# Kernel tuning notes

Hardware: AMD Instinct MI355X
Metric: run time of the kernel (lower is better)

## Reference

```python
import jax, jax.numpy as jnp
import numpy as np

LN_EPS = 1e-5

def setup_inputs() -> dict:
    key = jax.random.key(0)
    ks = jax.random.split(key, 12)
    B, S, D = 4, 2048, 1024
    s = 1.0 / np.sqrt(D)
    return {
        "query": jax.random.normal(ks[0], (B, S, D), jnp.float32),
        "key_in": jax.random.normal(ks[1], (B, S, D), jnp.float32),
        "value": jax.random.normal(ks[2], (B, S, D), jnp.float32),
        "Wq": jax.random.normal(ks[3], (D, D), jnp.float32) * s,
        "bq": jax.random.normal(ks[4], (D,), jnp.float32) * s,
        "Wk": jax.random.normal(ks[5], (D, D), jnp.float32) * s,
        "bk": jax.random.normal(ks[6], (D,), jnp.float32) * s,
        "Wv": jax.random.normal(ks[7], (D, D), jnp.float32) * s,
        "bv": jax.random.normal(ks[8], (D,), jnp.float32) * s,
        "gamma": jnp.ones((D,), jnp.float32),
        "beta": jnp.zeros((D,), jnp.float32),
    }

def reference(query, key_in, value, Wq, bq, Wk, bk, Wv, bv, gamma, beta):
    # Linear projections (torch Linear: x @ W^T + b; here W stored as [in,out])
    q = jnp.einsum('bsd,df->bsf', query, Wq) + bq
    k = jnp.einsum('bsd,df->bsf', key_in, Wk) + bk
    v = jnp.einsum('bsd,df->bsf', value, Wv) + bv
    # Attention: note NO 1/sqrt(d) scaling, single head (faithful to source)
    attn = jnp.einsum('bqd,bkd->bqk', q, k)          # [B,S,S]
    probs = jax.nn.softmax(attn, axis=-1)
    result = jnp.einsum('bqk,bkd->bqd', probs, v)     # [B,S,D]
    # Residual + LayerNorm
    x = result + query
    mu = jnp.mean(x, axis=-1, keepdims=True)
    var = jnp.mean((x - mu) ** 2, axis=-1, keepdims=True)
    return (x - mu) * jax.lax.rsqrt(var + LN_EPS) * gamma + beta
```

## Files before the change

### kernel.cpp

```cpp
#include <hip/hip_runtime.h>
#include <hip/hip_bf16.h>
#include <cstdint>


typedef unsigned short u16;
typedef unsigned int   u32;
typedef _Float16 f16;
typedef f16   f16x8  __attribute__((ext_vector_type(8)));
typedef f16   f16x4  __attribute__((ext_vector_type(4)));
typedef float f32x4  __attribute__((ext_vector_type(4)));

#define DEV __device__ __forceinline__

DEV void gld_lds16(const f16* g, char* l){
  __builtin_amdgcn_global_load_lds(
      (const __attribute__((address_space(1))) u32*)(uintptr_t)g,
      (__attribute__((address_space(3))) u32*)(u32)(uintptr_t)l, 16, 0, 0);
}

#define MFMA_(av, bv, ci, cj) \
  acc[ci][cj] = __builtin_amdgcn_mfma_f32_16x16x32_f16(av, bv, acc[ci][cj], 0, 0, 0)

DEV void gemm_core(const f16* __restrict__ A, int lda,
                   const f16* __restrict__ B, int ldb,
                   int nt, char* smem, f32x4 (&acc)[8][4])
{
  const int tid  = threadIdx.x;
  const int lane = tid & 63;
  const int wv   = tid >> 6;
  const int wm   = wv >> 2, wn = wv & 3;
  const int lr   = lane & 15, lq = lane >> 4;

  const int ob0 = tid * 16;
  const int ob1 = ob0 + 8192;
  const int r0  = ob0 >> 7, r1 = ob1 >> 7;
  const int sl0 = ((ob0 >> 4) & 7) ^ (r0 & 7);
  const int sl1 = ((ob1 >> 4) & 7) ^ (r1 & 7);
  const f16* src[8];
  src[0] = A + (size_t)r0 * lda + sl0 * 8;
  src[1] = A + (size_t)r1 * lda + sl1 * 8;
  src[2] = B + (size_t)r0 * ldb + sl0 * 8;
  src[3] = B + (size_t)r1 * ldb + sl1 * 8;
  src[4] = A + (size_t)(128 + r0) * lda + sl0 * 8;
  src[5] = A + (size_t)(128 + r1) * lda + sl1 * 8;
  src[6] = B + (size_t)(128 + r0) * ldb + sl0 * 8;
  src[7] = B + (size_t)(128 + r1) * ldb + sl1 * 8;

  const int rA  = (wm * 16 + lr) << 7;
  const int rB  = (wn * 16 + lr) << 7;
  const int sk0 = ((lq ^ (lane & 7)) << 4);
  const int sk1 = (((4 | lq) ^ (lane & 7)) << 4);

#pragma unroll
  for (int i = 0; i < 8; i++)
#pragma unroll
    for (int j = 0; j < 4; j++) acc[i][j] = (f32x4){0.f, 0.f, 0.f, 0.f};

  gld_lds16(src[0], smem +     0 + ob0); src[0] += 64;
  gld_lds16(src[1], smem +     0 + ob1); src[1] += 64;
  gld_lds16(src[2], smem + 32768 + ob0); src[2] += 64;
  gld_lds16(src[3], smem + 32768 + ob1); src[3] += 64;
  gld_lds16(src[4], smem + 16384 + ob0); src[4] += 64;
  gld_lds16(src[5], smem + 16384 + ob1); src[5] += 64;
  gld_lds16(src[6], smem + 49152 + ob0); src[6] += 64;
  gld_lds16(src[7], smem + 49152 + ob1); src[7] += 64;

  for (int t = 0; t < nt; ++t){
    char* bufc  = smem + ((t & 1) << 16);
    char* stash = smem + (((t & 1) ^ 1) << 16);
    const bool more = (t + 1 < nt);

    f16x8 a0[4], a1[4], b0[2], b1[2], b2[2], b3[2];

    if (more){ gld_lds16(src[0], stash + 0 + ob0); src[0] += 64; }
    if (more) asm volatile("s_waitcnt vmcnt(5)\ns_barrier" ::: "memory");
    else      asm volatile("s_waitcnt vmcnt(4)\ns_barrier" ::: "memory");
#pragma unroll
    for (int i = 0; i < 4; i++) a0[i] = *(const f16x8*)(bufc + (i << 12) + rA + sk0);
    b0[0] = *(const f16x8*)(bufc + 32768 +    0 + rB + sk0);
    b0[1] = *(const f16x8*)(bufc + 32768 + 8192 + rB + sk0);
    __builtin_amdgcn_s_setprio(1);
#pragma unroll
    for (int i = 0; i < 4; i++){ MFMA_(a0[i], b0[0], i, 0); MFMA_(a0[i], b0[1], i, 1); }
    __builtin_amdgcn_s_setprio(0);

    if (more){ gld_lds16(src[1], stash + 0 + ob1); src[1] += 64; }
#pragma unroll
    for (int i = 0; i < 4; i++) a1[i] = *(const f16x8*)(bufc + (i << 12) + rA + sk1);
    b1[0] = *(const f16x8*)(bufc + 32768 +    0 + rB + sk1);
    b1[1] = *(const f16x8*)(bufc + 32768 + 8192 + rB + sk1);
    __builtin_amdgcn_s_setprio(1);
#pragma unroll
    for (int i = 0; i < 4; i++){ MFMA_(a1[i], b1[0], i, 0); MFMA_(a1[i], b1[1], i, 1); }
    __builtin_amdgcn_s_setprio(0);

    if (more){ gld_lds16(src[2], stash + 32768 + ob0); src[2] += 64; }
    if (more) asm volatile("s_waitcnt vmcnt(3)\ns_barrier" ::: "memory");
    else      asm volatile("s_waitcnt vmcnt(0)\ns_barrier" ::: "memory");
    b2[0] = *(const f16x8*)(bufc + 49152 +    0 + rB + sk0);
    b2[1] = *(const f16x8*)(bufc + 49152 + 8192 + rB + sk0);
    __builtin_amdgcn_s_setprio(1);
#pragma unroll
    for (int i = 0; i < 4; i++){ MFMA_(a0[i], b2[0], i, 2); MFMA_(a0[i], b2[1], i, 3); }
    __builtin_amdgcn_s_setprio(0);

    if (more){ gld_lds16(src[3], stash + 32768 + ob1); src[3] += 64; }
    b3[0] = *(const f16x8*)(bufc + 49152 +    0 + rB + sk1);
    b3[1] = *(const f16x8*)(bufc + 49152 + 8192 + rB + sk1);
    __builtin_amdgcn_s_setprio(1);
#pragma unroll
    for (int i = 0; i < 4; i++){ MFMA_(a1[i], b3[0], i, 2); MFMA_(a1[i], b3[1], i, 3); }
    __builtin_amdgcn_s_setprio(0);

    if (more){ gld_lds16(src[4], stash + 16384 + ob0); src[4] += 64; }
#pragma unroll
    for (int i = 0; i < 4; i++) a0[i] = *(const f16x8*)(bufc + 16384 + (i << 12) + rA + sk0);
    __builtin_amdgcn_s_setprio(1);
#pragma unroll
    for (int i = 0; i < 4; i++){ MFMA_(a0[i], b0[0], 4 + i, 0); MFMA_(a0[i], b0[1], 4 + i, 1); }
    __builtin_amdgcn_s_setprio(0);

    if (more){ gld_lds16(src[5], stash + 16384 + ob1); src[5] += 64; }
#pragma unroll
    for (int i = 0; i < 4; i++) a1[i] = *(const f16x8*)(bufc + 16384 + (i << 12) + rA + sk1);
    __builtin_amdgcn_s_setprio(1);
#pragma unroll
    for (int i = 0; i < 4; i++){ MFMA_(a1[i], b1[0], 4 + i, 0); MFMA_(a1[i], b1[1], 4 + i, 1); }
    __builtin_amdgcn_s_setprio(0);

    if (more){ gld_lds16(src[6], stash + 49152 + ob0); src[6] += 64; }
    __builtin_amdgcn_s_setprio(1);
#pragma unroll
    for (int i = 0; i < 4; i++){ MFMA_(a0[i], b2[0], 4 + i, 2); MFMA_(a0[i], b2[1], 4 + i, 3); }
    __builtin_amdgcn_s_setprio(0);

    if (more){ gld_lds16(src[7], stash + 49152 + ob1); src[7] += 64; }
    __builtin_amdgcn_s_setprio(1);
#pragma unroll
    for (int i = 0; i < 4; i++){ MFMA_(a1[i], b3[0], 4 + i, 2); MFMA_(a1[i], b3[1], 4 + i, 3); }
    __builtin_amdgcn_s_setprio(0);
  }
}

__global__ __launch_bounds__(512, 2) void proj8p(
    const f16* __restrict__ xq, const f16* __restrict__ xk, const f16* __restrict__ xv,
    const f16* __restrict__ wq, const f16* __restrict__ wk, const f16* __restrict__ wv,
    const float* __restrict__ bq, const float* __restrict__ bk, const float* __restrict__ bv,
    f16* __restrict__ oq, f16* __restrict__ ok, f16* __restrict__ ovT)
{
  __shared__ char smem[131072];
  const int z  = blockIdx.z;
  const int m0 = blockIdx.y * 256, n0 = blockIdx.x * 256;
  const f16* A = (z == 0 ? xq : z == 1 ? xk : xv) + (size_t)m0 * 1024;
  const f16* B = (z == 0 ? wq : z == 1 ? wk : wv) + (size_t)n0 * 1024;
  const float* bias = (z == 0 ? bq : z == 1 ? bk : bv);

  f32x4 acc[8][4];
  gemm_core(A, 1024, B, 1024, 16, smem, acc);

  const int lane = threadIdx.x & 63;
  const int wv_  = threadIdx.x >> 6;
  const int wm = wv_ >> 2, wn = wv_ & 3;
  const int lr = lane & 15, rj = (lane >> 4) * 4;

  if (z < 2){
    f16* o = z ? ok : oq;
#pragma unroll
    for (int i = 0; i < 8; i++)
#pragma unroll
      for (int j = 0; j < 4; j++){
        int row = m0 + i * 32 + wm * 16 + rj;
        int col = n0 + j * 64 + wn * 16 + lr;
        float bvl = bias[col];
#pragma unroll
        for (int r = 0; r < 4; r++)
          o[(size_t)(row + r) * 1024 + col] = (f16)(acc[i][j][r] + bvl);
      }
  } else {
#pragma unroll
    for (int i = 0; i < 8; i++)
#pragma unroll
      for (int j = 0; j < 4; j++){
        int row = m0 + i * 32 + wm * 16 + rj;
        int col = n0 + j * 64 + wn * 16 + lr;
        float bvl = bias[col];
        f16x4 tv;
#pragma unroll
        for (int r = 0; r < 4; r++) tv[r] = (f16)(acc[i][j][r] + bvl);
        *(f16x4*)(ovT + (size_t)col * 8192 + row) = tv;
      }
  }
}

__global__ __launch_bounds__(512, 2) void qk8p(
    const f16* __restrict__ q, const f16* __restrict__ k, float* __restrict__ Sout)
{
  __shared__ char smem[131072];
  const int z  = blockIdx.z;
  const int m0 = blockIdx.y * 256, n0 = blockIdx.x * 256;
  const f16* A = q + (size_t)z * 2048 * 1024 + (size_t)m0 * 1024;
  const f16* B = k + (size_t)z * 2048 * 1024 + (size_t)n0 * 1024;

  f32x4 acc[8][4];
  gemm_core(A, 1024, B, 1024, 16, smem, acc);

  const int lane = threadIdx.x & 63;
  const int wv_  = threadIdx.x >> 6;
  const int wm = wv_ >> 2, wn = wv_ & 3;
  const int lr = lane & 15, rj = (lane >> 4) * 4;
  float* o = Sout + (size_t)z * 2048 * 2048;
#pragma unroll
  for (int i = 0; i < 8; i++)
#pragma unroll
    for (int j = 0; j < 4; j++){
      int row = m0 + i * 32 + wm * 16 + rj;
      int col = n0 + j * 64 + wn * 16 + lr;
#pragma unroll
      for (int r = 0; r < 4; r++)
        o[(size_t)(row + r) * 2048 + col] = acc[i][j][r];
    }
}

__global__ __launch_bounds__(512, 2) void pv8p(
    const f16* __restrict__ P, const f16* __restrict__ vT, float* __restrict__ O)
{
  __shared__ char smem[131072];
  const int z  = blockIdx.z;
  const int zb = z >> 1, h = z & 1;
  const int m0 = blockIdx.y * 256, n0 = blockIdx.x * 256;
  const f16* A = P  + (size_t)zb * 2048 * 2048 + (size_t)m0 * 2048 + h * 1024;
  const f16* B = vT + (size_t)n0 * 8192 + (size_t)zb * 2048 + h * 1024;

  f32x4 acc[8][4];
  gemm_core(A, 2048, B, 8192, 16, smem, acc);

  const int lane = threadIdx.x & 63;
  const int wv_  = threadIdx.x >> 6;
  const int wm = wv_ >> 2, wn = wv_ & 3;
  const int lr = lane & 15, rj = (lane >> 4) * 4;
  float* o = O + (size_t)h * 8388608 + (size_t)zb * 2048 * 1024;
#pragma unroll
  for (int i = 0; i < 8; i++)
#pragma unroll
    for (int j = 0; j < 4; j++){
      int row = m0 + i * 32 + wm * 16 + rj;
      int col = n0 + j * 64 + wn * 16 + lr;
#pragma unroll
      for (int r = 0; r < 4; r++)
        o[(size_t)(row + r) * 1024 + col] = acc[i][j][r];
    }
}

__global__ __launch_bounds__(256) void cvt_f32_f16(const float* __restrict__ x,
                                                   f16* __restrict__ y, int n){
  int i = (blockIdx.x * 256 + threadIdx.x) * 8;
  if (i >= n) return;
  float4 a = *(const float4*)(x + i);
  float4 b = *(const float4*)(x + i + 4);
  f16x8 v;
  v[0]=(f16)a.x; v[1]=(f16)a.y; v[2]=(f16)a.z; v[3]=(f16)a.w;
  v[4]=(f16)b.x; v[5]=(f16)b.y; v[6]=(f16)b.z; v[7]=(f16)b.w;
  *(f16x8*)(y + i) = v;
}

__global__ __launch_bounds__(256) void transpose_cvt_w(const float* __restrict__ W,
                                                       f16* __restrict__ T, int D){
  __shared__ float t[32][33];
  int tx = threadIdx.x & 31, ty = threadIdx.x >> 5;
  int bx = blockIdx.x * 32, by = blockIdx.y * 32;
#pragma unroll
  for (int j = 0; j < 4; j++) t[ty + j*8][tx] = W[(size_t)(by + ty + j*8) * D + bx + tx];
  __syncthreads();
#pragma unroll
  for (int j = 0; j < 4; j++){
    float v = t[tx][ty + j*8];
    T[(size_t)(bx + ty + j*8) * D + by + tx] = (f16)v;
  }
}

DEV float wred_max(float v){
#pragma unroll
  for (int o = 32; o; o >>= 1) v = fmaxf(v, __shfl_xor(v, o));
  return v;
}
DEV float wred_sum(float v){
#pragma unroll
  for (int o = 32; o; o >>= 1) v += __shfl_xor(v, o);
  return v;
}

__global__ __launch_bounds__(256) void softmax_rows(const float* __restrict__ S, f16* __restrict__ P){
  const int row = blockIdx.x;
  const int tid = threadIdx.x;
  const float* x = S + (size_t)row * 2048 + tid * 8;
  f16* p = P + (size_t)row * 2048 + tid * 8;
  float4 a = *(const float4*)x, b = *(const float4*)(x + 4);
  float v[8] = {a.x, a.y, a.z, a.w, b.x, b.y, b.z, b.w};
  __shared__ float red[4];

  float m = v[0];
#pragma unroll
  for (int j = 1; j < 8; j++) m = fmaxf(m, v[j]);
  m = wred_max(m);
  if ((tid & 63) == 0) red[tid >> 6] = m;
  __syncthreads();
  m = fmaxf(fmaxf(red[0], red[1]), fmaxf(red[2], red[3]));

  float s = 0.f;
#pragma unroll
  for (int j = 0; j < 8; j++){ v[j] = __expf(v[j] - m); s += v[j]; }
  s = wred_sum(s);
  __syncthreads();
  if ((tid & 63) == 0) red[tid >> 6] = s;
  __syncthreads();
  s = red[0] + red[1] + red[2] + red[3];

  float inv = 1.f / s;
  f16x8 o;
#pragma unroll
  for (int j = 0; j < 8; j++) o[j] = (f16)(v[j] * inv);
  *(f16x8*)p = o;
}

__global__ __launch_bounds__(256) void resid_ln2(const float* __restrict__ O0,
                                                 const float* __restrict__ O1,
                                                 const float* __restrict__ query,
                                                 const float* __restrict__ gamma,
                                                 const float* __restrict__ beta,
                                                 float* __restrict__ out){
  const int row = blockIdx.x;
  const int tid = threadIdx.x;
  const size_t base = (size_t)row * 1024 + tid * 4;
  float4 o4 = *(const float4*)(O0 + base);
  float4 p4 = *(const float4*)(O1 + base);
  float4 q4 = *(const float4*)(query + base);
  float x[4] = {o4.x + p4.x + q4.x, o4.y + p4.y + q4.y,
                o4.z + p4.z + q4.z, o4.w + p4.w + q4.w};
  float s = 0.f, ss = 0.f;
#pragma unroll
  for (int j = 0; j < 4; j++){ s += x[j]; ss += x[j] * x[j]; }

  __shared__ float red[4];
  s = wred_sum(s);
  if ((tid & 63) == 0) red[tid >> 6] = s;
  __syncthreads();
  s = red[0] + red[1] + red[2] + red[3];
  ss = wred_sum(ss);
  __syncthreads();
  if ((tid & 63) == 0) red[tid >> 6] = ss;
  __syncthreads();
  ss = red[0] + red[1] + red[2] + red[3];

  float mu = s * (1.f / 1024.f);
  float var = ss * (1.f / 1024.f) - mu * mu;
  float rs = rsqrtf(var + 1e-5f);
  float4 g4 = *(const float4*)(gamma + tid * 4);
  float4 b4 = *(const float4*)(beta + tid * 4);
  float4 r;
  r.x = (x[0] - mu) * rs * g4.x + b4.x;
  r.y = (x[1] - mu) * rs * g4.y + b4.y;
  r.z = (x[2] - mu) * rs * g4.z + b4.z;
  r.w = (x[3] - mu) * rs * g4.w + b4.w;
  *(float4*)(out + base) = r;
}

extern "C" void kernel_launch(void* const* d_in, const int* in_sizes, int n_in,
                              void* d_out, int out_size, void* d_ws, size_t ws_size,
                              hipStream_t stream){
  const float* query  = (const float*)d_in[0];
  const float* key_in = (const float*)d_in[1];
  const float* value  = (const float*)d_in[2];
  const float* Wq = (const float*)d_in[3];
  const float* bq = (const float*)d_in[4];
  const float* Wk = (const float*)d_in[5];
  const float* bk = (const float*)d_in[6];
  const float* Wv = (const float*)d_in[7];
  const float* bv = (const float*)d_in[8];
  const float* gamma = (const float*)d_in[9];
  const float* beta  = (const float*)d_in[10];

  const int B = 4, S = 2048, D = 1024;
  const int M = B * S;
  const size_t MB = 1ull << 20;
  char* ws = (char*)d_ws;

  f16* qf16 = (f16*)(ws + 0);
  f16* kf16 = (f16*)(ws + 16 * MB);
  f16* vT   = (f16*)(ws + 32 * MB);
  f16* wt_q = (f16*)(ws + 48 * MB);
  f16* wt_k = (f16*)(ws + 50 * MB);
  f16* wt_v = (f16*)(ws + 52 * MB);
  float* Obuf = (float*)(ws + 54 * MB);
  f16* xq   = (f16*)(ws + 118 * MB);
  f16* xk   = (f16*)(ws + 134 * MB);
  f16* xv   = (f16*)(ws + 150 * MB);
  float* Sbuf = (float*)(ws + 118 * MB);
  f16*   Pbuf = (f16*)(ws + 182 * MB);

  dim3 blk(256);
  const int nElem = M * D;

  cvt_f32_f16<<<nElem / 2048, blk, 0, stream>>>(query,  xq, nElem);
  cvt_f32_f16<<<nElem / 2048, blk, 0, stream>>>(key_in, xk, nElem);
  cvt_f32_f16<<<nElem / 2048, blk, 0, stream>>>(value,  xv, nElem);

  dim3 tg(32, 32);
  transpose_cvt_w<<<tg, blk, 0, stream>>>(Wq, wt_q, D);
  transpose_cvt_w<<<tg, blk, 0, stream>>>(Wk, wt_k, D);
  transpose_cvt_w<<<tg, blk, 0, stream>>>(Wv, wt_v, D);

  proj8p<<<dim3(4, 32, 3), dim3(512), 0, stream>>>(xq, xk, xv, wt_q, wt_k, wt_v,
                                                   bq, bk, bv, qf16, kf16, vT);

  qk8p<<<dim3(8, 8, 4), dim3(512), 0, stream>>>(qf16, kf16, Sbuf);

  softmax_rows<<<M, blk, 0, stream>>>(Sbuf, Pbuf);

  pv8p<<<dim3(4, 8, 8), dim3(512), 0, stream>>>(Pbuf, vT, Obuf);

  resid_ln2<<<M, blk, 0, stream>>>(Obuf, Obuf + 8388608, query, gamma, beta, (float*)d_out);
}
```

Measured before the change: 209.0 us.

## Swizzle GEMM block order across XCDs, peel last k-tile, merge prep launches

Each GEMM kernel now remaps its linear block id with an XCD-aware swizzle, so consecutive logical tiles land on the same chiplet and share L2 reuse of A/B panels. The k-loop body is templated on whether a prefetch follows, and the last iteration is peeled so the runtime 'more' branches drop out of the hot loop. The three f32->f16 convert launches and the three weight-transpose launches are each merged into one launch with a z dimension, which cuts launch overhead. The swizzle assumes the block count divides evenly by 8.

```diff
diff --git a/kernel.cpp b/kernel.cpp
--- a/kernel.cpp
+++ b/kernel.cpp
@@ -18,8 +18,90 @@
       (__attribute__((address_space(3))) u32*)(u32)(uintptr_t)l, 16, 0, 0);
 }
 
+DEV int swz_lid(){
+  int lid = (blockIdx.z * gridDim.y + blockIdx.y) * gridDim.x + blockIdx.x;
+  int cpx = (gridDim.x * gridDim.y * gridDim.z) >> 3;
+  return (lid & 7) * cpx + (lid >> 3);
+}
+
 #define MFMA_(av, bv, ci, cj) \
   acc[ci][cj] = __builtin_amdgcn_mfma_f32_16x16x32_f16(av, bv, acc[ci][cj], 0, 0, 0)
+
+template<bool MORE>
+DEV void ktile_body(const f16* (&src)[8], char* bufc, char* stash,
+                    int ob0, int ob1, int rA, int rB, int sk0, int sk1,
+                    f32x4 (&acc)[8][4])
+{
+  f16x8 a0[4], a1[4], b0[2], b1[2], b2[2], b3[2];
+
+  if (MORE){ gld_lds16(src[0], stash + 0 + ob0); src[0] += 64; }
+  if (MORE) asm volatile("s_waitcnt vmcnt(5)\ns_barrier" ::: "memory");
+  else      asm volatile("s_waitcnt vmcnt(4)\ns_barrier" ::: "memory");
+#pragma unroll
+  for (int i = 0; i < 4; i++) a0[i] = *(const f16x8*)(bufc + (i << 12) + rA + sk0);
+  b0[0] = *(const f16x8*)(bufc + 32768 +    0 + rB + sk0);
+  b0[1] = *(const f16x8*)(bufc + 32768 + 8192 + rB + sk0);
+  __builtin_amdgcn_s_setprio(1);
+#pragma unroll
+  for (int i = 0; i < 4; i++){ MFMA_(a0[i], b0[0], i, 0); MFMA_(a0[i], b0[1], i, 1); }
+  __builtin_amdgcn_s_setprio(0);
+
+  if (MORE){ gld_lds16(src[1], stash + 0 + ob1); src[1] += 64; }
+#pragma unroll
+  for (int i = 0; i < 4; i++) a1[i] = *(const f16x8*)(bufc + (i << 12) + rA + sk1);
+  b1[0] = *(const f16x8*)(bufc + 32768 +    0 + rB + sk1);
+  b1[1] = *(const f16x8*)(bufc + 32768 + 8192 + rB + sk1);
+  __builtin_amdgcn_s_setprio(1);
+#pragma unroll
+  for (int i = 0; i < 4; i++){ MFMA_(a1[i], b1[0], i, 0); MFMA_(a1[i], b1[1], i, 1); }
+  __builtin_amdgcn_s_setprio(0);
+
+  if (MORE){ gld_lds16(src[2], stash + 32768 + ob0); src[2] += 64; }
+  if (MORE) asm volatile("s_waitcnt vmcnt(3)\ns_barrier" ::: "memory");
+  else      asm volatile("s_waitcnt vmcnt(0)\ns_barrier" ::: "memory");
+  b2[0] = *(const f16x8*)(bufc + 49152 +    0 + rB + sk0);
+  b2[1] = *(const f16x8*)(bufc + 49152 + 8192 + rB + sk0);
+  __builtin_amdgcn_s_setprio(1);
+#pragma unroll
+  for (int i = 0; i < 4; i++){ MFMA_(a0[i], b2[0], i, 2); MFMA_(a0[i], b2[1], i, 3); }
+  __builtin_amdgcn_s_setprio(0);
+
+  if (MORE){ gld_lds16(src[3], stash + 32768 + ob1); src[3] += 64; }
+  b3[0] = *(const f16x8*)(bufc + 49152 +    0 + rB + sk1);
+  b3[1] = *(const f16x8*)(bufc + 49152 + 8192 + rB + sk1);
+  __builtin_amdgcn_s_setprio(1);
+#pragma unroll
+  for (int i = 0; i < 4; i++){ MFMA_(a1[i], b3[0], i, 2); MFMA_(a1[i], b3[1], i, 3); }
+  __builtin_amdgcn_s_setprio(0);
+
+  if (MORE){ gld_lds16(src[4], stash + 16384 + ob0); src[4] += 64; }
+#pragma unroll
+  for (int i = 0; i < 4; i++) a0[i] = *(const f16x8*)(bufc + 16384 + (i << 12) + rA + sk0);
+  __builtin_amdgcn_s_setprio(1);
+#pragma unroll
+  for (int i = 0; i < 4; i++){ MFMA_(a0[i], b0[0], 4 + i, 0); MFMA_(a0[i], b0[1], 4 + i, 1); }
+  __builtin_amdgcn_s_setprio(0);
+
+  if (MORE){ gld_lds16(src[5], stash + 16384 + ob1); src[5] += 64; }
+#pragma unroll
+  for (int i = 0; i < 4; i++) a1[i] = *(const f16x8*)(bufc + 16384 + (i << 12) + rA + sk1);
+  __builtin_amdgcn_s_setprio(1);
+#pragma unroll
+  for (int i = 0; i < 4; i++){ MFMA_(a1[i], b1[0], 4 + i, 0); MFMA_(a1[i], b1[1], 4 + i, 1); }
+  __builtin_amdgcn_s_setprio(0);
+
+  if (MORE){ gld_lds16(src[6], stash + 49152 + ob0); src[6] += 64; }
+  __builtin_amdgcn_s_setprio(1);
+#pragma unroll
+  for (int i = 0; i < 4; i++){ MFMA_(a0[i], b2[0], 4 + i, 2); MFMA_(a0[i], b2[1], 4 + i, 3); }
+  __builtin_amdgcn_s_setprio(0);
+
+  if (MORE){ gld_lds16(src[7], stash + 49152 + ob1); src[7] += 64; }
+  __builtin_amdgcn_s_setprio(1);
+#pragma unroll
+  for (int i = 0; i < 4; i++){ MFMA_(a1[i], b3[0], 4 + i, 2); MFMA_(a1[i], b3[1], 4 + i, 3); }
+  __builtin_amdgcn_s_setprio(0);
+}
 
 DEV void gemm_core(const f16* __restrict__ A, int lda,
                    const f16* __restrict__ B, int ldb,
@@ -65,80 +147,15 @@
   gld_lds16(src[6], smem + 49152 + ob0); src[6] += 64;
   gld_lds16(src[7], smem + 49152 + ob1); src[7] += 64;
 
-  for (int t = 0; t < nt; ++t){
+  for (int t = 0; t < nt - 1; ++t){
     char* bufc  = smem + ((t & 1) << 16);
     char* stash = smem + (((t & 1) ^ 1) << 16);
-    const bool more = (t + 1 < nt);
-
-    f16x8 a0[4], a1[4], b0[2], b1[2], b2[2], b3[2];
-
-    if (more){ gld_lds16(src[0], stash + 0 + ob0); src[0] += 64; }
-    if (more) asm volatile("s_waitcnt vmcnt(5)\ns_barrier" ::: "memory");
-    else      asm volatile("s_waitcnt vmcnt(4)\ns_barrier" ::: "memory");
-#pragma unroll
-    for (int i = 0; i < 4; i++) a0[i] = *(const f16x8*)(bufc + (i << 12) + rA + sk0);
-    b0[0] = *(const f16x8*)(bufc + 32768 +    0 + rB + sk0);
-    b0[1] = *(const f16x8*)(bufc + 32768 + 8192 + rB + sk0);
-    __builtin_amdgcn_s_setprio(1);
-#pragma unroll
-    for (int i = 0; i < 4; i++){ MFMA_(a0[i], b0[0], i, 0); MFMA_(a0[i], b0[1], i, 1); }
-    __builtin_amdgcn_s_setprio(0);
-
-    if (more){ gld_lds16(src[1], stash + 0 + ob1); src[1] += 64; }
-#pragma unroll
-    for (int i = 0; i < 4; i++) a1[i] = *(const f16x8*)(bufc + (i << 12) + rA + sk1);
-    b1[0] = *(const f16x8*)(bufc + 32768 +    0 + rB + sk1);
-    b1[1] = *(const f16x8*)(bufc + 32768 + 8192 + rB + sk1);
-    __builtin_amdgcn_s_setprio(1);
-#pragma unroll
-    for (int i = 0; i < 4; i++){ MFMA_(a1[i], b1[0], i, 0); MFMA_(a1[i], b1[1], i, 1); }
-    __builtin_amdgcn_s_setprio(0);
-
-    if (more){ gld_lds16(src[2], stash + 32768 + ob0); src[2] += 64; }
-    if (more) asm volatile("s_waitcnt vmcnt(3)\ns_barrier" ::: "memory");
-    else      asm volatile("s_waitcnt vmcnt(0)\ns_barrier" ::: "memory");
-    b2[0] = *(const f16x8*)(bufc + 49152 +    0 + rB + sk0);
-    b2[1] = *(const f16x8*)(bufc + 49152 + 8192 + rB + sk0);
-    __builtin_amdgcn_s_setprio(1);
-#pragma unroll
-    for (int i = 0; i < 4; i++){ MFMA_(a0[i], b2[0], i, 2); MFMA_(a0[i], b2[1], i, 3); }
-    __builtin_amdgcn_s_setprio(0);
-
-    if (more){ gld_lds16(src[3], stash + 32768 + ob1); src[3] += 64; }
-    b3[0] = *(const f16x8*)(bufc + 49152 +    0 + rB + sk1);
-    b3[1] = *(const f16x8*)(bufc + 49152 + 8192 + rB + sk1);
-    __builtin_amdgcn_s_setprio(1);
-#pragma unroll
-    for (int i = 0; i < 4; i++){ MFMA_(a1[i], b3[0], i, 2); MFMA_(a1[i], b3[1], i, 3); }
-    __builtin_amdgcn_s_setprio(0);
-
-    if (more){ gld_lds16(src[4], stash + 16384 + ob0); src[4] += 64; }
-#pragma unroll
-    for (int i = 0; i < 4; i++) a0[i] = *(const f16x8*)(bufc + 16384 + (i << 12) + rA + sk0);
-    __builtin_amdgcn_s_setprio(1);
-#pragma unroll
-    for (int i = 0; i < 4; i++){ MFMA_(a0[i], b0[0], 4 + i, 0); MFMA_(a0[i], b0[1], 4 + i, 1); }
-    __builtin_amdgcn_s_setprio(0);
-
-    if (more){ gld_lds16(src[5], stash + 16384 + ob1); src[5] += 64; }
-#pragma unroll
-    for (int i = 0; i < 4; i++) a1[i] = *(const f16x8*)(bufc + 16384 + (i << 12) + rA + sk1);
-    __builtin_amdgcn_s_setprio(1);
-#pragma unroll
-    for (int i = 0; i < 4; i++){ MFMA_(a1[i], b1[0], 4 + i, 0); MFMA_(a1[i], b1[1], 4 + i, 1); }
-    __builtin_amdgcn_s_setprio(0);
-
-    if (more){ gld_lds16(src[6], stash + 49152 + ob0); src[6] += 64; }
-    __builtin_amdgcn_s_setprio(1);
-#pragma unroll
-    for (int i = 0; i < 4; i++){ MFMA_(a0[i], b2[0], 4 + i, 2); MFMA_(a0[i], b2[1], 4 + i, 3); }
-    __builtin_amdgcn_s_setprio(0);
-
-    if (more){ gld_lds16(src[7], stash + 49152 + ob1); src[7] += 64; }
-    __builtin_amdgcn_s_setprio(1);
-#pragma unroll
-    for (int i = 0; i < 4; i++){ MFMA_(a1[i], b3[0], 4 + i, 2); MFMA_(a1[i], b3[1], 4 + i, 3); }
-    __builtin_amdgcn_s_setprio(0);
+    ktile_body<true>(src, bufc, stash, ob0, ob1, rA, rB, sk0, sk1, acc);
+  }
+  {
+    char* bufc  = smem + (((nt - 1) & 1) << 16);
+    char* stash = smem + ((((nt - 1) & 1) ^ 1) << 16);
+    ktile_body<false>(src, bufc, stash, ob0, ob1, rA, rB, sk0, sk1, acc);
   }
 }
 
@@ -149,8 +166,9 @@
     f16* __restrict__ oq, f16* __restrict__ ok, f16* __restrict__ ovT)
 {
   __shared__ char smem[131072];
-  const int z  = blockIdx.z;
-  const int m0 = blockIdx.y * 256, n0 = blockIdx.x * 256;
+  const int s  = swz_lid();
+  const int bx = s & 3, by = (s >> 2) & 31, z = s >> 7;
+  const int m0 = by * 256, n0 = bx * 256;
   const f16* A = (z == 0 ? xq : z == 1 ? xk : xv) + (size_t)m0 * 1024;
   const f16* B = (z == 0 ? wq : z == 1 ? wk : wv) + (size_t)n0 * 1024;
   const float* bias = (z == 0 ? bq : z == 1 ? bk : bv);
@@ -196,8 +214,9 @@
     const f16* __restrict__ q, const f16* __restrict__ k, float* __restrict__ Sout)
 {
   __shared__ char smem[131072];
-  const int z  = blockIdx.z;
-  const int m0 = blockIdx.y * 256, n0 = blockIdx.x * 256;
+  const int s  = swz_lid();
+  const int bx = s & 7, by = (s >> 3) & 7, z = s >> 6;
+  const int m0 = by * 256, n0 = bx * 256;
   const f16* A = q + (size_t)z * 2048 * 1024 + (size_t)m0 * 1024;
   const f16* B = k + (size_t)z * 2048 * 1024 + (size_t)n0 * 1024;
 
@@ -225,9 +244,10 @@
     const f16* __restrict__ P, const f16* __restrict__ vT, float* __restrict__ O)
 {
   __shared__ char smem[131072];
-  const int z  = blockIdx.z;
+  const int s  = swz_lid();
+  const int bx = s & 3, by = (s >> 2) & 7, z = s >> 5;
   const int zb = z >> 1, h = z & 1;
-  const int m0 = blockIdx.y * 256, n0 = blockIdx.x * 256;
+  const int m0 = by * 256, n0 = bx * 256;
   const f16* A = P  + (size_t)zb * 2048 * 2048 + (size_t)m0 * 2048 + h * 1024;
   const f16* B = vT + (size_t)n0 * 8192 + (size_t)zb * 2048 + h * 1024;
 
@@ -251,10 +271,13 @@
     }
 }
 
-__global__ __launch_bounds__(256) void cvt_f32_f16(const float* __restrict__ x,
-                                                   f16* __restrict__ y, int n){
+__global__ __launch_bounds__(256) void cvt3_f32_f16(
+    const float* __restrict__ x0, const float* __restrict__ x1, const float* __restrict__ x2,
+    f16* __restrict__ y0, f16* __restrict__ y1, f16* __restrict__ y2){
+  const int z = blockIdx.y;
+  const float* x = z == 0 ? x0 : z == 1 ? x1 : x2;
+  f16* y = z == 0 ? y0 : z == 1 ? y1 : y2;
   int i = (blockIdx.x * 256 + threadIdx.x) * 8;
-  if (i >= n) return;
   float4 a = *(const float4*)(x + i);
   float4 b = *(const float4*)(x + i + 4);
   f16x8 v;
@@ -263,8 +286,12 @@
   *(f16x8*)(y + i) = v;
 }
 
-__global__ __launch_bounds__(256) void transpose_cvt_w(const float* __restrict__ W,
-                                                       f16* __restrict__ T, int D){
+__global__ __launch_bounds__(256) void transpose3_cvt_w(
+    const float* __restrict__ W0, const float* __restrict__ W1, const float* __restrict__ W2,
+    f16* __restrict__ T0, f16* __restrict__ T1, f16* __restrict__ T2, int D){
+  const int z = blockIdx.z;
+  const float* W = z == 0 ? W0 : z == 1 ? W1 : W2;
+  f16* T = z == 0 ? T0 : z == 1 ? T1 : T2;
   __shared__ float t[32][33];
   int tx = threadIdx.x & 31, ty = threadIdx.x >> 5;
   int bx = blockIdx.x * 32, by = blockIdx.y * 32;
@@ -400,14 +427,8 @@
   dim3 blk(256);
   const int nElem = M * D;
 
-  cvt_f32_f16<<<nElem / 2048, blk, 0, stream>>>(query,  xq, nElem);
-  cvt_f32_f16<<<nElem / 2048, blk, 0, stream>>>(key_in, xk, nElem);
-  cvt_f32_f16<<<nElem / 2048, blk, 0, stream>>>(value,  xv, nElem);
-
-  dim3 tg(32, 32);
-  transpose_cvt_w<<<tg, blk, 0, stream>>>(Wq, wt_q, D);
-  transpose_cvt_w<<<tg, blk, 0, stream>>>(Wk, wt_k, D);
-  transpose_cvt_w<<<tg, blk, 0, stream>>>(Wv, wt_v, D);
+  cvt3_f32_f16<<<dim3(nElem / 2048, 3), blk, 0, stream>>>(query, key_in, value, xq, xk, xv);
+  transpose3_cvt_w<<<dim3(32, 32, 3), blk, 0, stream>>>(Wq, Wk, Wv, wt_q, wt_k, wt_v, D);
 
   proj8p<<<dim3(4, 32, 3), dim3(512), 0, stream>>>(xq, xk, xv, wt_q, wt_k, wt_v,
                                                    bq, bk, bv, qf16, kf16, vT);
```

Result: faster. 195.6 us (-6.4%).
